# Kernel tuning notes

Measured on AMD Instinct MI355X. Metric: run time of the kernel, lower is better.

Reference implementation:

```python
import jax, jax.numpy as jnp
import numpy as np
from itertools import combinations

Nt, Nrf, Nk, FEAT, BATCH = 64, 4, 8, 512, 1024
Ng = Nt // Nk                      # 8
_MAX = len(list(combinations(range(Ng), Nrf)))  # 70
CSETSIZE = int(2 ** np.floor(np.log2(_MAX)))    # 64
SQRT_NRF = np.float32(np.sqrt(Nrf))


def _generate_antenna_selection_set(num_target):
    """Max-hamming-distance antenna selection set (numpy, matches torch code)."""
    combs = list(combinations(range(Ng), Nrf))
    maxSize = len(combs)
    globalSet = np.zeros((maxSize, Nt, Nrf), np.float32)
    for i, act in enumerate(combs):
        for j, a in enumerate(act):
            globalSet[i, a * Nk:a * Nk + Nk, j] = 1.0
    gsum = globalSet.sum(-1)  # (maxSize, Nt)
    selectSet = np.zeros((num_target, Nt, Nrf), np.float32)
    available = []
    for idx in range(num_target):
        if len(available) == 0:
            available = list(range(maxSize))
        if idx == 0:
            hd = np.zeros(len(available))
        else:
            sel = selectSet[:idx].sum(-1)            # (idx, Nt)
            cand = gsum[np.array(available)]          # (nAvail, Nt)
            hd = (sel[None, :, :] != cand[:, None, :]).sum(axis=(1, 2))
        sid = available[int(np.argmax(hd))]
        selectSet[idx] = globalSet[sid]
        available.remove(sid)
    return selectSet


def setup_inputs() -> dict:
    key = jax.random.key(0)
    ks = jax.random.split(key, 7)
    s = 1.0 / np.sqrt(FEAT)
    DDIM = CSETSIZE * Nrf * Nrf
    return {
        "x": jax.random.normal(ks[0], (BATCH, FEAT), jnp.float32),
        "W_A": jax.random.normal(ks[1], (Nt, FEAT), jnp.float32) * s,
        "b_A": jax.random.normal(ks[2], (Nt,), jnp.float32) * s,
        "W_Dr": jax.random.normal(ks[3], (DDIM, FEAT), jnp.float32) * s,
        "b_Dr": jax.random.normal(ks[4], (DDIM,), jnp.float32) * s,
        "W_Di": jax.random.normal(ks[5], (DDIM, FEAT), jnp.float32) * s,
        "b_Di": jax.random.normal(ks[6], (DDIM,), jnp.float32) * s,
        "CSet": jnp.asarray(_generate_antenna_selection_set(CSETSIZE)),
    }


def reference(x, W_A, b_A, W_Dr, b_Dr, W_Di, b_Di, CSet):
    B = x.shape[0]
    theta = x @ W_A.T + b_A                          # (B, Nt)
    cosT, sinT = jnp.cos(theta), jnp.sin(theta)
    eye = jnp.eye(Nt, dtype=x.dtype)
    A_real = (cosT[:, :, None] * eye)[:, None]       # (B, 1, Nt, Nt) diag-embed
    A_imag = (sinT[:, :, None] * eye)[:, None]
    D_real = (x @ W_Dr.T + b_Dr).reshape(B, CSETSIZE, Nrf, Nrf)
    D_imag = (x @ W_Di.T + b_Di).reshape(B, CSETSIZE, Nrf, Nrf)
    # diag(cos) @ C == row-scale of C (identical math to the dense matmul)
    ArC = cosT[:, None, :, None] * CSet[None]        # (B, CSetSize, Nt, Nrf)
    AiC = sinT[:, None, :, None] * CSet[None]
    ArCDr = ArC @ D_real
    ArCDi = ArC @ D_imag
    AiCDr = AiC @ D_real
    AiCDi = AiC @ D_imag
    V_real = ArCDr - AiCDi                           # (B, CSetSize, Nt, Nrf)
    V_imag = ArCDi + AiCDr
    V_F = jnp.sqrt(jnp.sum(V_real ** 2 + V_imag ** 2, axis=(2, 3)))
    V_F = V_F[:, :, None, None]
    D_real_n = SQRT_NRF * D_real / V_F
    D_imag_n = SQRT_NRF * D_imag / V_F
    return (A_real, A_imag, D_real_n, D_imag_n, CSet)
```

## Files before the change

### kernel.cpp

```cpp
#include <hip/hip_runtime.h>
#include <math.h>

#define BATCH 1024
#define FEAT  512
#define NT    64
#define DDIM  1024

typedef __attribute__((ext_vector_type(8))) short  short8;
typedef __attribute__((ext_vector_type(4))) short  short4v;
typedef __attribute__((ext_vector_type(4))) float  floatx4;

__device__ __forceinline__ unsigned short bf16rne(float f) {
    unsigned int u = __float_as_uint(f);
    return (unsigned short)((u + 0x7fffu + ((u >> 16) & 1u)) >> 16);
}
__device__ __forceinline__ short4v pack4(const float4 a) {
    short4v r;
    r[0] = (short)bf16rne(a.x); r[1] = (short)bf16rne(a.y);
    r[2] = (short)bf16rne(a.z); r[3] = (short)bf16rne(a.w);
    return r;
}


__global__ __launch_bounds__(256) void k1_gemm(
    const float* __restrict__ x,
    const float* __restrict__ W_A,  const float* __restrict__ b_A,
    const float* __restrict__ W_Dr, const float* __restrict__ b_Dr,
    const float* __restrict__ W_Di, const float* __restrict__ b_Di,
    float* __restrict__ out, float* __restrict__ theta_ws)
{
    __shared__ __align__(16) unsigned short As[64][40];
    __shared__ __align__(16) unsigned short Bs[64][40];

    const int bid  = blockIdx.x;
    const int tid  = threadIdx.x;
    const int lane = tid & 63;
    const int wv   = tid >> 6;
    const int ln   = lane & 15;
    const int quad = lane >> 4;

    const int f = tid & 7;
    const int r = tid >> 3;

    const bool isD = (bid < 512);
    int row0, woff, ldsn0, ldsn1;
    const float *arow0, *arow1, *brow0, *brow1;

    if (isD) {
        const int by = bid >> 5;
        const int bx = bid & 31;
        row0 = by * 64;
        woff = bx * 32;
        brow0 = W_Dr + (size_t)(woff + r) * FEAT;
        brow1 = W_Di + (size_t)(woff + r) * FEAT;
        ldsn0 = (r >> 4) * 32 + (r & 15);
        ldsn1 = (r >> 4) * 32 + 16 + (r & 15);
    } else {
        const int by = bid - 512;
        row0 = by * 64;
        woff = 0;
        brow0 = W_A + (size_t)r * FEAT;
        brow1 = W_A + (size_t)(r + 32) * FEAT;
        ldsn0 = r;
        ldsn1 = r + 32;
    }
    arow0 = x + (size_t)(row0 + r) * FEAT;
    arow1 = x + (size_t)(row0 + r + 32) * FEAT;

    float4 pa0 = *(const float4*)(arow0 + f * 4);
    float4 pa1 = *(const float4*)(arow1 + f * 4);
    float4 pb0 = *(const float4*)(brow0 + f * 4);
    float4 pb1 = *(const float4*)(brow1 + f * 4);

    floatx4 acc[4] = {{0,0,0,0},{0,0,0,0},{0,0,0,0},{0,0,0,0}};

    #pragma unroll 1
    for (int it = 0; it < 16; ++it) {
        __syncthreads();
        *(short4v*)&As[r][f * 4]        = pack4(pa0);
        *(short4v*)&As[r + 32][f * 4]   = pack4(pa1);
        *(short4v*)&Bs[ldsn0][f * 4]    = pack4(pb0);
        *(short4v*)&Bs[ldsn1][f * 4]    = pack4(pb1);
        __syncthreads();

        if (it < 15) {
            const int ko = (it + 1) * 32 + f * 4;
            pa0 = *(const float4*)(arow0 + ko);
            pa1 = *(const float4*)(arow1 + ko);
            pb0 = *(const float4*)(brow0 + ko);
            pb1 = *(const float4*)(brow1 + ko);
        }

        const short8 a = *(const short8*)&As[wv * 16 + ln][quad * 8];
        #pragma unroll
        for (int t = 0; t < 4; ++t) {
            const short8 b = *(const short8*)&Bs[t * 16 + ln][quad * 8];
            acc[t] = __builtin_amdgcn_mfma_f32_16x16x32_bf16(a, b, acc[t], 0, 0, 0);
        }
    }

    if (isD) {
        const size_t drn = (size_t)2 * BATCH * 4096;
        const size_t din = drn + (size_t)BATCH * DDIM;
        #pragma unroll
        for (int p = 0; p < 2; ++p) {
            const int colg = woff + p * 16 + ln;
            const float br = b_Dr[colg];
            const float bi = b_Di[colg];
            float dr[4], di[4], ps[4];
            #pragma unroll
            for (int i = 0; i < 4; ++i) {
                dr[i] = acc[2 * p][i] + br;
                di[i] = acc[2 * p + 1][i] + bi;
                ps[i] = dr[i] * dr[i] + di[i] * di[i];
            }
            #pragma unroll
            for (int i = 0; i < 4; ++i) {
                ps[i] += __shfl_xor(ps[i], 1);
                ps[i] += __shfl_xor(ps[i], 2);
                ps[i] += __shfl_xor(ps[i], 4);
                ps[i] += __shfl_xor(ps[i], 8);
            }
            #pragma unroll
            for (int i = 0; i < 4; ++i) {
                const float scale = 2.0f / sqrtf(8.0f * ps[i]);
                const size_t row_g = (size_t)(row0 + wv * 16 + quad * 4 + i);
                out[drn + row_g * DDIM + colg] = dr[i] * scale;
                out[din + row_g * DDIM + colg] = di[i] * scale;
            }
        }
    } else {
        #pragma unroll
        for (int t = 0; t < 4; ++t) {
            const int colg = t * 16 + ln;
            const float ba = b_A[colg];
            #pragma unroll
            for (int i = 0; i < 4; ++i) {
                const int row_g = row0 + wv * 16 + quad * 4 + i;
                theta_ws[row_g * NT + colg] = acc[t][i] + ba;
            }
        }
    }
}

__global__ __launch_bounds__(256) void k2_fill(
    const float* __restrict__ theta_ws,
    const float* __restrict__ cset,
    float* __restrict__ out)
{
    const int beta = blockIdx.x;
    const int tid  = threadIdx.x;

    if (beta < 4096) {
        const int b  = beta >> 2;
        const int rg = beta & 3;
        const int t  = rg * 16 + (tid >> 4);
        const int j  = tid & 15;

        const float th = theta_ws[b * NT + t];
        float s, c;
        sincosf(th, &s, &c);

        float4 vr = {0.f, 0.f, 0.f, 0.f};
        float4 vi = {0.f, 0.f, 0.f, 0.f};
        if ((t >> 2) == j) {
            ((float*)&vr)[t & 3] = c;
            ((float*)&vi)[t & 3] = s;
        }
        const size_t off = (size_t)b * 4096 + t * 64 + j * 4;
        *(float4*)(out + off) = vr;
        *(float4*)(out + (size_t)BATCH * 4096 + off) = vi;
    } else {
        const int cb = beta - 4096;
        const size_t base = (size_t)2 * BATCH * 4096 + (size_t)2 * BATCH * DDIM;
        ((float4*)(out + base))[cb * 256 + tid] = ((const float4*)cset)[cb * 256 + tid];
    }
}

extern "C" void kernel_launch(void* const* d_in, const int* in_sizes, int n_in,
                              void* d_out, int out_size, void* d_ws, size_t ws_size,
                              hipStream_t stream) {
    const float* x    = (const float*)d_in[0];
    const float* W_A  = (const float*)d_in[1];
    const float* b_A  = (const float*)d_in[2];
    const float* W_Dr = (const float*)d_in[3];
    const float* b_Dr = (const float*)d_in[4];
    const float* W_Di = (const float*)d_in[5];
    const float* b_Di = (const float*)d_in[6];
    const float* CSet = (const float*)d_in[7];
    float* out   = (float*)d_out;
    float* theta = (float*)d_ws;

    k1_gemm<<<528, 256, 0, stream>>>(x, W_A, b_A, W_Dr, b_Dr, W_Di, b_Di,
                                     out, theta);
    k2_fill<<<4112, 256, 0, stream>>>(theta, CSet, out);
}
```

Before: 112.5 us.

## Pre-convert operands to swizzled bf16 tiles and stream via global_load_lds double buffer

```diff
diff --git a/kernel.cpp b/kernel.cpp
--- a/kernel.cpp
+++ b/kernel.cpp
@@ -7,101 +7,139 @@
 #define DDIM  1024
 
 typedef __attribute__((ext_vector_type(8))) short  short8;
-typedef __attribute__((ext_vector_type(4))) short  short4v;
 typedef __attribute__((ext_vector_type(4))) float  floatx4;
+
+#define AIMG_OFF  0
+#define BIMG_OFF  1048576
+#define THETA_OFF 3276800
 
 __device__ __forceinline__ unsigned short bf16rne(float f) {
     unsigned int u = __float_as_uint(f);
     return (unsigned short)((u + 0x7fffu + ((u >> 16) & 1u)) >> 16);
 }
-__device__ __forceinline__ short4v pack4(const float4 a) {
-    short4v r;
-    r[0] = (short)bf16rne(a.x); r[1] = (short)bf16rne(a.y);
-    r[2] = (short)bf16rne(a.z); r[3] = (short)bf16rne(a.w);
-    return r;
-}
-
+
+__device__ __forceinline__ void gld16(const unsigned char* g, unsigned char* l) {
+    __builtin_amdgcn_global_load_lds(
+        (const __attribute__((address_space(1))) unsigned int*)g,
+        (__attribute__((address_space(3))) unsigned int*)l, 16, 0, 0);
+}
+
+__global__ __launch_bounds__(256) void k0_convert(
+    const float* __restrict__ x,
+    const float* __restrict__ W_A,
+    const float* __restrict__ W_Dr,
+    const float* __restrict__ W_Di,
+    unsigned char* __restrict__ ws)
+{
+    unsigned short* aimg = (unsigned short*)(ws + AIMG_OFF);
+    unsigned short* bimg = (unsigned short*)(ws + BIMG_OFF);
+    const int gtid = blockIdx.x * 256 + threadIdx.x;
+
+    for (int idx = gtid; idx < 200704; idx += 65536) {
+        const float* src;
+        unsigned short* dst;
+        if (idx < 65536) {
+            const int rt = idx >> 12, kb = (idx >> 9) & 7;
+            const int r  = (idx >> 3) & 63, c = idx & 7;
+            src = x + ((size_t)(rt * 64 + r) * FEAT + kb * 64 + c * 8);
+            dst = aimg + ((rt * 8 + kb) * 4096 + r * 64 + ((c ^ (r & 7)) * 8));
+        } else {
+            const int j  = idx - 65536;
+            const int ct = j >> 12, kb = (j >> 9) & 7;
+            const int n  = (j >> 3) & 63, c = j & 7;
+            const float* wrow;
+            if (ct < 32) {
+                const int g = n >> 5, h = (n >> 4) & 1, pos = n & 15;
+                wrow = (h ? W_Di : W_Dr) + (size_t)(ct * 32 + g * 16 + pos) * FEAT;
+            } else {
+                wrow = W_A + (size_t)n * FEAT;
+            }
+            src = wrow + kb * 64 + c * 8;
+            dst = bimg + ((ct * 8 + kb) * 4096 + n * 64 + ((c ^ (n & 7)) * 8));
+        }
+        const float4 v0 = *(const float4*)src;
+        const float4 v1 = *(const float4*)(src + 4);
+        short8 o;
+        o[0] = (short)bf16rne(v0.x); o[1] = (short)bf16rne(v0.y);
+        o[2] = (short)bf16rne(v0.z); o[3] = (short)bf16rne(v0.w);
+        o[4] = (short)bf16rne(v1.x); o[5] = (short)bf16rne(v1.y);
+        o[6] = (short)bf16rne(v1.z); o[7] = (short)bf16rne(v1.w);
+        *(short8*)dst = o;
+    }
+}
 
 __global__ __launch_bounds__(256) void k1_gemm(
-    const float* __restrict__ x,
-    const float* __restrict__ W_A,  const float* __restrict__ b_A,
-    const float* __restrict__ W_Dr, const float* __restrict__ b_Dr,
-    const float* __restrict__ W_Di, const float* __restrict__ b_Di,
+    const unsigned char* __restrict__ ws,
+    const float* __restrict__ b_A,
+    const float* __restrict__ b_Dr, const float* __restrict__ b_Di,
     float* __restrict__ out, float* __restrict__ theta_ws)
 {
-    __shared__ __align__(16) unsigned short As[64][40];
-    __shared__ __align__(16) unsigned short Bs[64][40];
+    __shared__ __align__(16) unsigned char smem[32768];
 
     const int bid  = blockIdx.x;
+    const int rt   = bid & 15;
+    const int ct   = bid >> 4;
     const int tid  = threadIdx.x;
     const int lane = tid & 63;
     const int wv   = tid >> 6;
     const int ln   = lane & 15;
     const int quad = lane >> 4;
-
-    const int f = tid & 7;
-    const int r = tid >> 3;
-
-    const bool isD = (bid < 512);
-    int row0, woff, ldsn0, ldsn1;
-    const float *arow0, *arow1, *brow0, *brow1;
-
-    if (isD) {
-        const int by = bid >> 5;
-        const int bx = bid & 31;
-        row0 = by * 64;
-        woff = bx * 32;
-        brow0 = W_Dr + (size_t)(woff + r) * FEAT;
-        brow1 = W_Di + (size_t)(woff + r) * FEAT;
-        ldsn0 = (r >> 4) * 32 + (r & 15);
-        ldsn1 = (r >> 4) * 32 + 16 + (r & 15);
-    } else {
-        const int by = bid - 512;
-        row0 = by * 64;
-        woff = 0;
-        brow0 = W_A + (size_t)r * FEAT;
-        brow1 = W_A + (size_t)(r + 32) * FEAT;
-        ldsn0 = r;
-        ldsn1 = r + 32;
-    }
-    arow0 = x + (size_t)(row0 + r) * FEAT;
-    arow1 = x + (size_t)(row0 + r + 32) * FEAT;
-
-    float4 pa0 = *(const float4*)(arow0 + f * 4);
-    float4 pa1 = *(const float4*)(arow1 + f * 4);
-    float4 pb0 = *(const float4*)(brow0 + f * 4);
-    float4 pb1 = *(const float4*)(brow1 + f * 4);
+    const int row0 = rt * 64;
+
+    const unsigned char* Atiles = ws + AIMG_OFF + (size_t)rt * 8 * 8192;
+    const unsigned char* Btiles = ws + BIMG_OFF + (size_t)ct * 8 * 8192;
+
+    const int g0 = (wv * 2 + 0) * 1024;
+    const int g1 = (wv * 2 + 1) * 1024;
+    const int lo = lane * 16;
 
     floatx4 acc[4] = {{0,0,0,0},{0,0,0,0},{0,0,0,0},{0,0,0,0}};
 
+    {
+        unsigned char* La = smem;
+        unsigned char* Lb = smem + 8192;
+        gld16(Atiles + g0 + lo, La + g0);
+        gld16(Atiles + g1 + lo, La + g1);
+        gld16(Btiles + g0 + lo, Lb + g0);
+        gld16(Btiles + g1 + lo, Lb + g1);
+    }
+
+    const int rowOffA = (wv * 16 + ln) * 128;
+    const int swz = ln & 7;
+    int cur = 0;
+
     #pragma unroll 1
-    for (int it = 0; it < 16; ++it) {
+    for (int kb = 0; kb < 8; ++kb) {
         __syncthreads();
-        *(short4v*)&As[r][f * 4]        = pack4(pa0);
-        *(short4v*)&As[r + 32][f * 4]   = pack4(pa1);
-        *(short4v*)&Bs[ldsn0][f * 4]    = pack4(pb0);
-        *(short4v*)&Bs[ldsn1][f * 4]    = pack4(pb1);
-        __syncthreads();
-
-        if (it < 15) {
-            const int ko = (it + 1) * 32 + f * 4;
-            pa0 = *(const float4*)(arow0 + ko);
-            pa1 = *(const float4*)(arow1 + ko);
-            pb0 = *(const float4*)(brow0 + ko);
-            pb1 = *(const float4*)(brow1 + ko);
-        }
-
-        const short8 a = *(const short8*)&As[wv * 16 + ln][quad * 8];
+        if (kb < 7) {
+            const unsigned char* At = Atiles + (kb + 1) * 8192;
+            const unsigned char* Bt = Btiles + (kb + 1) * 8192;
+            unsigned char* La = smem + (cur ^ 1) * 16384;
+            unsigned char* Lb = La + 8192;
+            gld16(At + g0 + lo, La + g0);
+            gld16(At + g1 + lo, La + g1);
+            gld16(Bt + g0 + lo, Lb + g0);
+            gld16(Bt + g1 + lo, Lb + g1);
+        }
+        const unsigned char* La = smem + cur * 16384;
+        const unsigned char* Lb = La + 8192;
         #pragma unroll
-        for (int t = 0; t < 4; ++t) {
-            const short8 b = *(const short8*)&Bs[t * 16 + ln][quad * 8];
-            acc[t] = __builtin_amdgcn_mfma_f32_16x16x32_bf16(a, b, acc[t], 0, 0, 0);
-        }
-    }
-
-    if (isD) {
+        for (int ks = 0; ks < 2; ++ks) {
+            const int ca = ((ks * 4 + quad) ^ swz) * 16;
+            const short8 a = *(const short8*)(La + rowOffA + ca);
+            #pragma unroll
+            for (int t = 0; t < 4; ++t) {
+                const short8 b = *(const short8*)(Lb + (t * 16 + ln) * 128 + ca);
+                acc[t] = __builtin_amdgcn_mfma_f32_16x16x32_bf16(a, b, acc[t], 0, 0, 0);
+            }
+        }
+        cur ^= 1;
+    }
+
+    if (ct < 32) {
         const size_t drn = (size_t)2 * BATCH * 4096;
         const size_t din = drn + (size_t)BATCH * DDIM;
+        const int woff = ct * 32;
         #pragma unroll
         for (int p = 0; p < 2; ++p) {
             const int colg = woff + p * 16 + ln;
@@ -188,10 +226,11 @@
     const float* W_Di = (const float*)d_in[5];
     const float* b_Di = (const float*)d_in[6];
     const float* CSet = (const float*)d_in[7];
-    float* out   = (float*)d_out;
-    float* theta = (float*)d_ws;
-
-    k1_gemm<<<528, 256, 0, stream>>>(x, W_A, b_A, W_Dr, b_Dr, W_Di, b_Di,
-                                     out, theta);
+    float* out = (float*)d_out;
+    unsigned char* ws = (unsigned char*)d_ws;
+    float* theta = (float*)(ws + THETA_OFF);
+
+    k0_convert<<<256, 256, 0, stream>>>(x, W_A, W_Dr, W_Di, ws);
+    k1_gemm<<<528, 256, 0, stream>>>(ws, b_A, b_Dr, b_Di, out, theta);
     k2_fill<<<4112, 256, 0, stream>>>(theta, CSet, out);
 }
```

Measured after the change: 107.1 us. 4.8% less time.
